# Performance work log

Measured on AMD Instinct MI355X. Metric: run time of the kernel, lower is better.

The kernel has to match this reference:

```python
import jax, jax.numpy as jnp
import numpy as np

RATIO = 0.25
RADIUS = 0.2
NSAMPLE = 32


def fps(xyz, S):
    """Farthest point sampling. xyz: [B,N,3] -> indices [B,S] (int32)."""
    B, N, _ = xyz.shape

    def step(carry, _):
        min_d, last_idx = carry  # [B,N], [B]
        centroid = jnp.take_along_axis(xyz, last_idx[:, None, None], axis=1)  # [B,1,3]
        d = jnp.sum((xyz - centroid) ** 2, axis=-1)  # [B,N]
        min_d = jnp.minimum(min_d, d)
        nxt = jnp.argmax(min_d, axis=-1).astype(jnp.int32)
        return (min_d, nxt), last_idx

    init = (jnp.full((B, N), 1e10, xyz.dtype), jnp.zeros((B,), jnp.int32))
    _, idxs = jax.lax.scan(step, init, None, length=S)  # [S,B]
    return idxs.T  # [B,S]


def ball_query(radius, nsample, xyz, new_xyz):
    """xyz: [B,N,3], new_xyz: [B,S,3] -> group idx [B,S,nsample] (int32)."""
    B, S, _ = new_xyz.shape
    N = xyz.shape[1]
    sqd = jnp.sum((new_xyz[:, :, None, :] - xyz[:, None, :, :]) ** 2, axis=-1)  # [B,S,N]
    idx = jnp.broadcast_to(jnp.arange(N, dtype=jnp.int32), (B, S, N))
    idx = jnp.where(sqd > radius * radius, N, idx)
    idx = jnp.sort(idx, axis=-1)[:, :, :nsample]  # first nsample in-ball ids (ascending)
    first = idx[:, :, :1]
    idx = jnp.where(idx == N, first, idx)  # pad empties with first neighbor
    return idx


def reference(xyz, features, W1, b1, W2, b2):
    B, N, _ = xyz.shape
    S = int(N * RATIO)
    fps_idx = fps(xyz, S)  # [B,S]
    new_xyz = jnp.take_along_axis(xyz, fps_idx[:, :, None], axis=1)  # [B,S,3]
    grp_idx = ball_query(RADIUS, NSAMPLE, xyz, new_xyz)  # [B,S,K]
    batch = jnp.arange(B, dtype=jnp.int32)[:, None, None]
    new_points = features[batch, grp_idx]  # [B,S,K,D]
    # shared MLP (1x1 Conv2d equivalents) + ReLU
    h = jax.nn.relu(jnp.einsum('bskd,ed->bske', new_points, W1) + b1)
    h = jax.nn.relu(jnp.einsum('bskd,ed->bske', h, W2) + b2)
    new_points_out = jnp.max(h, axis=2)  # max over group K -> [B,S,D']
    new_points_out = new_points_out.transpose(0, 2, 1)  # [B,D',S]
    new_xyz_out = new_xyz.transpose(0, 2, 1)  # [B,3,S]
    return new_xyz_out, new_points_out


def setup_inputs() -> dict:
    key = jax.random.key(0)
    k1, k2, k3, k4 = jax.random.split(key, 4)
    B, N, D = 16, 4096, 64
    xyz = jax.random.uniform(k1, (B, N, 3), dtype=jnp.float32)
    features = jax.random.normal(k2, (B, N, D), dtype=jnp.float32)
    W1 = jax.random.normal(k3, (64, 64), dtype=jnp.float32) * (1.0 / np.sqrt(64))
    b1 = jnp.zeros((64,), jnp.float32)
    W2 = jax.random.normal(k4, (128, 64), dtype=jnp.float32) * (1.0 / np.sqrt(64))
    b2 = jnp.zeros((128,), jnp.float32)
    return {"xyz": xyz, "features": features, "W1": W1, "b1": b1, "W2": W2, "b2": b2}
```

## Files before the change

### kernel.cpp

```cpp
#include <hip/hip_runtime.h>
#include <hip/hip_bf16.h>

#define BATCH 16
#define NPTS  4096
#define NSAMP 1024
#define KNB   32
#define DFEAT 64

#define THREADS  512
#define FPS_PPT  (NPTS / THREADS)
#define NWV      (THREADS / 64)
#define NWBLK    240
#define NWAVES   (NWBLK * NWV)
#define NTASK    (BATCH * NSAMP)
#define TAG_BASE 0xC0FFEE00u

template <int CTRL, int RMASK>
__device__ __forceinline__ void dpp_round(unsigned long long& key) {
    const int klo = (int)(unsigned)key;
    const int khi = (int)(unsigned)(key >> 32);
    const int tlo = __builtin_amdgcn_update_dpp(klo, klo, CTRL, RMASK, 0xF, false);
    const int thi = __builtin_amdgcn_update_dpp(khi, khi, CTRL, RMASK, 0xF, false);
    const unsigned long long tk =
        ((unsigned long long)(unsigned)thi << 32) | (unsigned)tlo;
    if (tk > key) key = tk;
}

__device__ __forceinline__ void pub_store(unsigned long long* p, unsigned long long v) {
    __hip_atomic_store(p, v, __ATOMIC_RELAXED, __HIP_MEMORY_SCOPE_AGENT);
}
__device__ __forceinline__ unsigned long long pub_load(const unsigned long long* p) {
    return __hip_atomic_load(p, __ATOMIC_RELAXED, __HIP_MEMORY_SCOPE_AGENT);
}

__device__ __forceinline__ void barrier_lds_only() {
    asm volatile("s_waitcnt lgkmcnt(0)" ::: "memory");
    __builtin_amdgcn_s_barrier();
}

__global__ __launch_bounds__(THREADS) void fused_kernel(
    const float* __restrict__ xyz, const float* __restrict__ features,
    const float* __restrict__ W1, const float* __restrict__ b1,
    const float* __restrict__ W2, const float* __restrict__ b2,
    float* __restrict__ out_xyz, float* __restrict__ out_pts,
    unsigned long long* __restrict__ pub) {

    __shared__ alignas(16) unsigned char smem[65536 + 12288 + 512];
    const int bid  = blockIdx.x;
    const int tid  = threadIdx.x;
    const int lane = tid & 63;
    const int wid  = tid >> 6;

    if (bid < BATCH) {
        float4* sc = (float4*)smem;
        float* stX = (float*)(smem + 65536);
        float* stY = stX + NSAMP;
        float* stZ = stY + NSAMP;
        unsigned long long* pw = (unsigned long long*)(smem + 65536 + 12288);

        float px[FPS_PPT], py[FPS_PPT], pz[FPS_PPT], md[FPS_PPT];
        const float* base = xyz + (size_t)bid * NPTS * 3;
#pragma unroll
        for (int j = 0; j < FPS_PPT; j++) {
            const int i = j * THREADS + tid;
            const float x = base[i * 3 + 0];
            const float y = base[i * 3 + 1];
            const float z = base[i * 3 + 2];
            sc[i] = make_float4(x, y, z, 0.0f);
            px[j] = x; py[j] = y; pz[j] = z;
            md[j] = 1e10f;
        }

        float cx = base[0], cy = base[1], cz = base[2];
        unsigned long long* pb = pub + (size_t)bid * NSAMP * 3;
        if (tid == 0) {
            stX[0] = cx; stY[0] = cy; stZ[0] = cz;
            pub_store(&pb[0], ((unsigned long long)__float_as_uint(cx) << 32) | (TAG_BASE + 0));
            pub_store(&pb[1], ((unsigned long long)__float_as_uint(cy) << 32) | (TAG_BASE + 0));
            pub_store(&pb[2], ((unsigned long long)__float_as_uint(cz) << 32) | (TAG_BASE + 0));
        }
        __syncthreads();

        for (int s = 1; s < NSAMP; s++) {
            float best = -1.0f;
            int   bj   = 0;
#pragma unroll
            for (int j = 0; j < FPS_PPT; j++) {
                const float dx = px[j] - cx;
                const float dy = py[j] - cy;
                const float dz = pz[j] - cz;
                const float d = __fadd_rn(__fadd_rn(__fmul_rn(dx, dx), __fmul_rn(dy, dy)),
                                          __fmul_rn(dz, dz));
                const float m = fminf(md[j], d);
                md[j] = m;
                if (m > best) { best = m; bj = j; }
            }
            const int bi = (bj << 9) | tid;
            unsigned long long key =
                ((unsigned long long)__float_as_uint(best) << 32) | (unsigned)(~bi);
            dpp_round<0x111, 0xF>(key);
            dpp_round<0x112, 0xF>(key);
            dpp_round<0x114, 0xF>(key);
            dpp_round<0x118, 0xF>(key);
            dpp_round<0x142, 0xA>(key);
            dpp_round<0x143, 0xC>(key);

            const int par = s & 1;
            if (lane == 63) pw[par * NWV + wid] = key;
            barrier_lds_only();
            const ulong2 p01 = *(const ulong2*)&pw[par * NWV + 0];
            const ulong2 p23 = *(const ulong2*)&pw[par * NWV + 2];
            const ulong2 p45 = *(const ulong2*)&pw[par * NWV + 4];
            const ulong2 p67 = *(const ulong2*)&pw[par * NWV + 6];
            unsigned long long bk = p01.x;
            if (p01.y > bk) bk = p01.y;
            if (p23.x > bk) bk = p23.x;
            if (p23.y > bk) bk = p23.y;
            if (p45.x > bk) bk = p45.x;
            if (p45.y > bk) bk = p45.y;
            if (p67.x > bk) bk = p67.x;
            if (p67.y > bk) bk = p67.y;
            const int bix = (int)(~(unsigned)bk);

            const float4 c = sc[bix];
            cx = c.x; cy = c.y; cz = c.z;
            if (tid == 0) {
                stX[s] = cx; stY[s] = cy; stZ[s] = cz;
                pub_store(&pb[3 * s + 0], ((unsigned long long)__float_as_uint(cx) << 32) | (TAG_BASE + s));
                pub_store(&pb[3 * s + 1], ((unsigned long long)__float_as_uint(cy) << 32) | (TAG_BASE + s));
                pub_store(&pb[3 * s + 2], ((unsigned long long)__float_as_uint(cz) << 32) | (TAG_BASE + s));
            }
        }

        __syncthreads();
        float* ob = out_xyz + (size_t)bid * 3 * NSAMP;
        for (int i = tid; i < NSAMP; i += THREADS) {
            ob[0 * NSAMP + i] = stX[i];
            ob[1 * NSAMP + i] = stY[i];
            ob[2 * NSAMP + i] = stZ[i];
        }
    } else {
        float (*xls)[KNB][DFEAT] = (float (*)[KNB][DFEAT])smem;
        float (*h1s)[DFEAT]      = (float (*)[DFEAT])(smem + 65536);
        int   (*gl)[KNB]         = (int (*)[KNB])(smem + 65536 + 2048);

        float w1r[64], w2ra[64], w2rb[64];
        {
            const float4* W1v = (const float4*)(W1 + (size_t)lane * 64);
            const float4* W2a = (const float4*)(W2 + (size_t)lane * 64);
            const float4* W2b = (const float4*)(W2 + (size_t)(lane + 64) * 64);
#pragma unroll
            for (int i = 0; i < 16; i++) {
                float4 v = W1v[i];
                w1r[4 * i] = v.x; w1r[4 * i + 1] = v.y; w1r[4 * i + 2] = v.z; w1r[4 * i + 3] = v.w;
                v = W2a[i];
                w2ra[4 * i] = v.x; w2ra[4 * i + 1] = v.y; w2ra[4 * i + 2] = v.z; w2ra[4 * i + 3] = v.w;
                v = W2b[i];
                w2rb[4 * i] = v.x; w2rb[4 * i + 1] = v.y; w2rb[4 * i + 2] = v.z; w2rb[4 * i + 3] = v.w;
            }
        }
        const float b1r  = b1[lane];
        const float b2ra = b2[lane];
        const float b2rb = b2[lane + 64];

        const int gwave = (bid - BATCH) * NWV + wid;
        for (int t = gwave; t < NTASK; t += NWAVES) {
            const int sq = t >> 4;
            const int b  = t & 15;

            const unsigned long long* pp = pub + ((size_t)b * NSAMP + sq) * 3;
            const unsigned exp_tag = TAG_BASE + sq;
            unsigned long long w0, w1, w2;
            for (;;) {
                w0 = pub_load(&pp[0]);
                w1 = pub_load(&pp[1]);
                w2 = pub_load(&pp[2]);
                if ((unsigned)w0 == exp_tag && (unsigned)w1 == exp_tag &&
                    (unsigned)w2 == exp_tag) break;
                __builtin_amdgcn_s_sleep(2);
            }
            const float cx = __uint_as_float((unsigned)(w0 >> 32));
            const float cy = __uint_as_float((unsigned)(w1 >> 32));
            const float cz = __uint_as_float((unsigned)(w2 >> 32));

            const float* base = xyz + (size_t)b * NPTS * 3;
            const float r2 = 0.04f;
            int cnt = 0;
            int firstCand = 0x7fffffff;
            for (int bp = 0; bp < NPTS && cnt < KNB; bp += 64) {
                const int p = bp + lane;
                const float dx = base[p * 3 + 0] - cx;
                const float dy = base[p * 3 + 1] - cy;
                const float dz = base[p * 3 + 2] - cz;
                const float d = __fadd_rn(__fadd_rn(__fmul_rn(dx, dx), __fmul_rn(dy, dy)),
                                          __fmul_rn(dz, dz));
                const bool ok = !(d > r2);
                const unsigned long long m = __ballot(ok);
                const int rank = cnt + (int)__popcll(m & ((1ull << lane) - 1ull));
                if (ok && rank < KNB) gl[wid][rank] = p;
                if (ok && rank == 0) firstCand = p;
                cnt += (int)__popcll(m);
            }
            const int found = cnt < KNB ? cnt : KNB;
            if (found < KNB) {
#pragma unroll
                for (int off = 32; off > 0; off >>= 1) {
                    const int o = __shfl_xor(firstCand, off);
                    firstCand = o < firstCand ? o : firstCand;
                }
                for (int r = found + lane; r < KNB; r += 64) gl[wid][r] = firstCand;
            }
            int gi = 0;
            if (lane < KNB) gi = gl[wid][lane];

            const float* fb = features + (size_t)b * NPTS * DFEAT;
            for (int k = 0; k < KNB; k++) {
                const int idxk = __shfl(gi, k);
                xls[wid][k][lane] = fb[(size_t)idxk * DFEAT + lane];
            }

            float m0 = 0.0f, m1 = 0.0f;
            for (int k = 0; k < KNB; k++) {
                float acc = b1r;
                const float4* xk = (const float4*)xls[wid][k];
#pragma unroll
                for (int i = 0; i < 16; i++) {
                    const float4 v = xk[i];
                    acc = fmaf(v.x, w1r[4 * i], acc);
                    acc = fmaf(v.y, w1r[4 * i + 1], acc);
                    acc = fmaf(v.z, w1r[4 * i + 2], acc);
                    acc = fmaf(v.w, w1r[4 * i + 3], acc);
                }
                h1s[wid][lane] = fmaxf(acc, 0.0f);
                float a0 = b2ra, a1 = b2rb;
                const float4* hv4 = (const float4*)h1s[wid];
#pragma unroll
                for (int i = 0; i < 16; i++) {
                    const float4 v = hv4[i];
                    a0 = fmaf(v.x, w2ra[4 * i], a0);
                    a0 = fmaf(v.y, w2ra[4 * i + 1], a0);
                    a0 = fmaf(v.z, w2ra[4 * i + 2], a0);
                    a0 = fmaf(v.w, w2ra[4 * i + 3], a0);
                    a1 = fmaf(v.x, w2rb[4 * i], a1);
                    a1 = fmaf(v.y, w2rb[4 * i + 1], a1);
                    a1 = fmaf(v.z, w2rb[4 * i + 2], a1);
                    a1 = fmaf(v.w, w2rb[4 * i + 3], a1);
                }
                m0 = fmaxf(m0, fmaxf(a0, 0.0f));
                m1 = fmaxf(m1, fmaxf(a1, 0.0f));
            }

            out_pts[(size_t)b * 128 * NSAMP + (size_t)lane * NSAMP + sq]        = m0;
            out_pts[(size_t)b * 128 * NSAMP + (size_t)(lane + 64) * NSAMP + sq] = m1;
        }
    }
}

extern "C" void kernel_launch(void* const* d_in, const int* in_sizes, int n_in,
                              void* d_out, int out_size, void* d_ws, size_t ws_size,
                              hipStream_t stream) {
    const float* xyz      = (const float*)d_in[0];
    const float* features = (const float*)d_in[1];
    const float* W1       = (const float*)d_in[2];
    const float* b1       = (const float*)d_in[3];
    const float* W2       = (const float*)d_in[4];
    const float* b2       = (const float*)d_in[5];

    float* out_xyz = (float*)d_out;
    float* out_pts = (float*)d_out + (size_t)BATCH * 3 * NSAMP;

    unsigned long long* pub = (unsigned long long*)d_ws;

    fused_kernel<<<BATCH + NWBLK, THREADS, 0, stream>>>(
        xyz, features, W1, b1, W2, b2, out_xyz, out_pts, pub);
}
```

Before: 680.9 us.

## Halve block size to 256 threads, double worker blocks, split FPS LDS layout

```diff
diff --git a/kernel.cpp b/kernel.cpp
--- a/kernel.cpp
+++ b/kernel.cpp
@@ -7,13 +7,24 @@
 #define KNB   32
 #define DFEAT 64
 
-#define THREADS  512
+#define THREADS  256
 #define FPS_PPT  (NPTS / THREADS)
 #define NWV      (THREADS / 64)
-#define NWBLK    240
+#define NWBLK    480
 #define NWAVES   (NWBLK * NWV)
 #define NTASK    (BATCH * NSAMP)
 #define TAG_BASE 0xC0FFEE00u
+
+#define SMEM_BYTES 61568
+#define FPS_SXY_OFF 0
+#define FPS_SZ_OFF  32768
+#define FPS_STX_OFF 49152
+#define FPS_STY_OFF 53248
+#define FPS_STZ_OFF 57344
+#define FPS_PW_OFF  61440
+#define WRK_XLS_OFF 0
+#define WRK_H1S_OFF 32768
+#define WRK_GL_OFF  33792
 
 template <int CTRL, int RMASK>
 __device__ __forceinline__ void dpp_round(unsigned long long& key) {
@@ -45,18 +56,19 @@
     float* __restrict__ out_xyz, float* __restrict__ out_pts,
     unsigned long long* __restrict__ pub) {
 
-    __shared__ alignas(16) unsigned char smem[65536 + 12288 + 512];
+    __shared__ alignas(16) unsigned char smem[SMEM_BYTES];
     const int bid  = blockIdx.x;
     const int tid  = threadIdx.x;
     const int lane = tid & 63;
     const int wid  = tid >> 6;
 
     if (bid < BATCH) {
-        float4* sc = (float4*)smem;
-        float* stX = (float*)(smem + 65536);
-        float* stY = stX + NSAMP;
-        float* stZ = stY + NSAMP;
-        unsigned long long* pw = (unsigned long long*)(smem + 65536 + 12288);
+        float2* sxy = (float2*)(smem + FPS_SXY_OFF);
+        float*  szl = (float*)(smem + FPS_SZ_OFF);
+        float*  stX = (float*)(smem + FPS_STX_OFF);
+        float*  stY = (float*)(smem + FPS_STY_OFF);
+        float*  stZ = (float*)(smem + FPS_STZ_OFF);
+        unsigned long long* pw = (unsigned long long*)(smem + FPS_PW_OFF);
 
         float px[FPS_PPT], py[FPS_PPT], pz[FPS_PPT], md[FPS_PPT];
         const float* base = xyz + (size_t)bid * NPTS * 3;
@@ -66,7 +78,8 @@
             const float x = base[i * 3 + 0];
             const float y = base[i * 3 + 1];
             const float z = base[i * 3 + 2];
-            sc[i] = make_float4(x, y, z, 0.0f);
+            sxy[i] = make_float2(x, y);
+            szl[i] = z;
             px[j] = x; py[j] = y; pz[j] = z;
             md[j] = 1e10f;
         }
@@ -95,7 +108,7 @@
                 md[j] = m;
                 if (m > best) { best = m; bj = j; }
             }
-            const int bi = (bj << 9) | tid;
+            const int bi = (bj << 8) | tid;
             unsigned long long key =
                 ((unsigned long long)__float_as_uint(best) << 32) | (unsigned)(~bi);
             dpp_round<0x111, 0xF>(key);
@@ -110,20 +123,15 @@
             barrier_lds_only();
             const ulong2 p01 = *(const ulong2*)&pw[par * NWV + 0];
             const ulong2 p23 = *(const ulong2*)&pw[par * NWV + 2];
-            const ulong2 p45 = *(const ulong2*)&pw[par * NWV + 4];
-            const ulong2 p67 = *(const ulong2*)&pw[par * NWV + 6];
             unsigned long long bk = p01.x;
             if (p01.y > bk) bk = p01.y;
             if (p23.x > bk) bk = p23.x;
             if (p23.y > bk) bk = p23.y;
-            if (p45.x > bk) bk = p45.x;
-            if (p45.y > bk) bk = p45.y;
-            if (p67.x > bk) bk = p67.x;
-            if (p67.y > bk) bk = p67.y;
             const int bix = (int)(~(unsigned)bk);
 
-            const float4 c = sc[bix];
-            cx = c.x; cy = c.y; cz = c.z;
+            const float2 cxy = sxy[bix];
+            const float  cz2 = szl[bix];
+            cx = cxy.x; cy = cxy.y; cz = cz2;
             if (tid == 0) {
                 stX[s] = cx; stY[s] = cy; stZ[s] = cz;
                 pub_store(&pb[3 * s + 0], ((unsigned long long)__float_as_uint(cx) << 32) | (TAG_BASE + s));
@@ -140,9 +148,9 @@
             ob[2 * NSAMP + i] = stZ[i];
         }
     } else {
-        float (*xls)[KNB][DFEAT] = (float (*)[KNB][DFEAT])smem;
-        float (*h1s)[DFEAT]      = (float (*)[DFEAT])(smem + 65536);
-        int   (*gl)[KNB]         = (int (*)[KNB])(smem + 65536 + 2048);
+        float (*xls)[KNB][DFEAT] = (float (*)[KNB][DFEAT])(smem + WRK_XLS_OFF);
+        float (*h1s)[DFEAT]      = (float (*)[DFEAT])(smem + WRK_H1S_OFF);
+        int   (*gl)[KNB]         = (int (*)[KNB])(smem + WRK_GL_OFF);
 
         float w1r[64], w2ra[64], w2rb[64];
         {
```

Measured after the change: 1.013 ms. 48.7% more time.
